# Optimization experiments

Hardware: AMD Instinct MI355X
Metric: run time of the kernel (lower is better)

## Reference

```python
import jax, jax.numpy as jnp
import numpy as np

BN_EPS = 1e-5


def setup_inputs() -> dict:
    N, E, D, L = 100000, 1200000, 64, 3
    key = jax.random.key(0)
    ks = jax.random.split(key, 6)
    x = jax.random.normal(ks[0], (N, D), dtype=jnp.float32)
    src = jax.random.randint(ks[1], (E,), 0, N, dtype=jnp.int32)
    dst = jax.random.randint(ks[2], (E,), 0, N, dtype=jnp.int32)
    W1 = jax.random.normal(ks[3], (L, D, D), dtype=jnp.float32) * 0.1
    W2 = jax.random.normal(ks[4], (L, D, D), dtype=jnp.float32) * 0.1
    b1 = jnp.zeros((L, D), jnp.float32)
    b2 = jnp.zeros((L, D), jnp.float32)
    bn_gamma = jnp.ones((L, D), jnp.float32)
    bn_beta = jnp.zeros((L, D), jnp.float32)
    bn_mean = jnp.zeros((L, D), jnp.float32)
    bn_var = jnp.ones((L, D), jnp.float32)
    return {"x": x, "src": src, "dst": dst, "W1": W1, "b1": b1,
            "bn_gamma": bn_gamma, "bn_beta": bn_beta, "bn_mean": bn_mean,
            "bn_var": bn_var, "W2": W2, "b2": b2}


def reference(x, src, dst, W1, b1, bn_gamma, bn_beta, bn_mean, bn_var, W2, b2):
    # GIN stack, eval mode (dropout is a no-op, BatchNorm uses running stats).
    N = x.shape[0]
    L = W1.shape[0]
    h = x
    jk_sum = jnp.zeros((N, W2.shape[-1]), x.dtype)
    for layer in range(L):  # small fixed layer loop
        # GINConv with eps=0: (1+eps)*x_i + sum_{j->i} x_j
        agg = jax.ops.segment_sum(h[src], dst, num_segments=N)  # [N, D]
        pre = h + agg
        # MLP: Linear -> BatchNorm1d (inference) -> ReLU -> Linear
        z = pre @ W1[layer] + b1[layer]
        z = bn_gamma[layer] * (z - bn_mean[layer]) * jax.lax.rsqrt(bn_var[layer] + BN_EPS) + bn_beta[layer]
        z = jax.nn.relu(z)
        h = z @ W2[layer] + b2[layer]
        if layer != L - 1:
            h = jax.nn.relu(h)  # inter-layer ReLU from the wrapper
        jk_sum = jk_sum + h  # JK='sum' over h_list[1:]
    return jk_sum
```

## Files before the change

kernel.cpp:

```cpp
#include <hip/hip_runtime.h>
#include <hip/hip_fp16.h>

#define NDIM 64
#define RS 68
#define MAXNB 512
#define CAP 6144
#define EBUF 352

typedef _Float16 h4 __attribute__((ext_vector_type(4)));
typedef float f4v __attribute__((ext_vector_type(4)));

__global__ __launch_bounds__(256) void prep_kernel(
    const float* __restrict__ x, __half* __restrict__ x16, int n4,
    const float* __restrict__ W1, const float* __restrict__ b1,
    const float* __restrict__ gamma, const float* __restrict__ beta,
    const float* __restrict__ mean, const float* __restrict__ var,
    const float* __restrict__ W2,
    _Float16* __restrict__ Wpk, float* __restrict__ b1f, int L)
{
    int bid = blockIdx.x;
    int t = threadIdx.x;
    if (bid < 2 * L) {
        int l = bid >> 1, m = bid & 1;
        const float* Wsrc = (m == 0 ? W1 : W2) + (size_t)l * 4096;
        if (m == 0 && t < 64) {
            float s = gamma[l * 64 + t] * rsqrtf(var[l * 64 + t] + 1e-5f);
            b1f[l * 64 + t] = (b1[l * 64 + t] - mean[l * 64 + t]) * s + beta[l * 64 + t];
        }
        int lane = t & 63;
        int c16 = lane & 15, kq = lane >> 4;
        for (int it = 0; it < 4; ++it) {
            int frag = it * 4 + (t >> 6);
            int ks = frag >> 2, ct = frag & 3;
            int col = ct * 16 + c16;
            int k0 = ks * 16 + kq * 4;
            float s = 1.f;
            if (m == 0) s = gamma[l * 64 + col] * rsqrtf(var[l * 64 + col] + 1e-5f);
            _Float16* dstp = Wpk + (((size_t)(l * 2 + m) * 16 + frag) * 64 + lane) * 8;
            for (int j = 0; j < 4; ++j) {
                float wv = Wsrc[(size_t)(k0 + j) * 64 + col] * s;
                _Float16 hi = (_Float16)wv;
                dstp[j] = hi;
                dstp[4 + j] = (_Float16)(wv - (float)hi);
            }
        }
        return;
    }
    int tid = (bid - 2 * L) * 256 + t;
    if (tid >= n4) return;
    float4 v = *(const float4*)(x + (size_t)tid * 4);
    __half2* dp = (__half2*)(x16 + (size_t)tid * 4);
    dp[0] = __floats2half2_rn(v.x, v.y);
    dp[1] = __floats2half2_rn(v.z, v.w);
}

__global__ __launch_bounds__(256) void bucket_scatter_kernel(
    const int* __restrict__ src, const int* __restrict__ dst,
    int* __restrict__ bcnt, unsigned int* __restrict__ packed, int E, int NBb)
{
    __shared__ int hist[MAXNB];
    __shared__ int sbase[MAXNB];
    for (int i = threadIdx.x; i < NBb; i += 256) hist[i] = 0;
    __syncthreads();
    int start = blockIdx.x * blockDim.x + threadIdx.x;
    int stride = gridDim.x * blockDim.x;
    for (int e = start; e < E; e += stride)
        atomicAdd(&hist[dst[e] >> 8], 1);
    __syncthreads();
    for (int i = threadIdx.x; i < NBb; i += 256) {
        int v = hist[i];
        sbase[i] = v ? (i * CAP + atomicAdd(&bcnt[i], v)) : 0;
    }
    __syncthreads();
    for (int i = threadIdx.x; i < NBb; i += 256) hist[i] = 0;
    __syncthreads();
    for (int e = start; e < E; e += stride) {
        int d = dst[e];
        int b = d >> 8;
        int r = atomicAdd(&hist[b], 1);
        packed[sbase[b] + r] = (unsigned)src[e] | ((unsigned)(d & 255) << 24);
    }
}

__global__ __launch_bounds__(256) void bucket_csr_kernel(
    const unsigned int* __restrict__ packed, const int* __restrict__ bcnt,
    int* __restrict__ ssrc, int* __restrict__ offs, int* __restrict__ ends, int N)
{
    __shared__ int hist[256], scan[256], cur[256];
    __shared__ int swbase;
    int b = blockIdx.x;
    int t = threadIdx.x;
    int partial = 0;
    for (int i = t; i < b; i += 256) partial += bcnt[i];
    scan[t] = partial;
    hist[t] = 0;
    __syncthreads();
    for (int d = 128; d > 0; d >>= 1) {
        if (t < d) scan[t] += scan[t + d];
        __syncthreads();
    }
    if (t == 0) swbase = scan[0];
    __syncthreads();
    int wbase = swbase;
    int cnt = bcnt[b];
    if (cnt > CAP) cnt = CAP;
    size_t rbase = (size_t)b * CAP;
    for (int i = t; i < cnt; i += 256)
        atomicAdd(&hist[packed[rbase + i] >> 24], 1);
    __syncthreads();
    int v = hist[t];
    scan[t] = v;
    __syncthreads();
    for (int d = 1; d < 256; d <<= 1) {
        int x = scan[t];
        int y = (t >= d) ? scan[t - d] : 0;
        __syncthreads();
        scan[t] = x + y;
        __syncthreads();
    }
    int e0 = wbase + scan[t] - v;
    cur[t] = e0;
    int node = b * 256 + t;
    if (node < N) { offs[node] = e0; ends[node] = e0 + v; }
    __syncthreads();
    for (int i = t; i < cnt; i += 256) {
        unsigned p = packed[rbase + i];
        int pos = atomicAdd(&cur[p >> 24], 1);
        ssrc[pos] = (int)(p & 0xFFFFFF);
    }
}

__device__ inline void add4(float4& a, const float4& v) {
    a.x += v.x; a.y += v.y; a.z += v.z; a.w += v.w;
}

__device__ inline void cvt_acc(uint4 u, float4& a0, float4& a1) {
    __half2 h0 = __builtin_bit_cast(__half2, u.x);
    __half2 h1 = __builtin_bit_cast(__half2, u.y);
    __half2 h2 = __builtin_bit_cast(__half2, u.z);
    __half2 h3 = __builtin_bit_cast(__half2, u.w);
    float2 f0 = __half22float2(h0), f1 = __half22float2(h1);
    float2 f2 = __half22float2(h2), f3 = __half22float2(h3);
    a0.x += f0.x; a0.y += f0.y; a0.z += f1.x; a0.w += f1.y;
    a1.x += f2.x; a1.y += f2.y; a1.z += f3.x; a1.w += f3.y;
}

__global__ __launch_bounds__(256, 7) void gin_layer_kernel(
    const __half* __restrict__ hin, __half* __restrict__ hout,
    float* __restrict__ jk,
    const int* __restrict__ offs, const int* __restrict__ ends,
    const int* __restrict__ ssrc,
    const _Float16* __restrict__ w1p, const _Float16* __restrict__ w2p,
    const float* __restrict__ b1f, const float* __restrict__ b2,
    int N, int relu_out, int first, int write_h)
{
    __shared__ float lds[64 * RS];
    __shared__ int ebuf_s[4 * EBUF];
    int t = threadIdx.x;
    int lane = t & 63;
    int w = t >> 6;
    int row0 = blockIdx.x * 64;
    int wrow0 = row0 + w * 16;
    if (wrow0 >= N) return;

    float* wtile = lds + (size_t)w * 16 * RS;
    int* ebuf = ebuf_s + w * EBUF;

    int offv = 0, endv = 0;
    if (lane < 16) {
        int node = wrow0 + lane;
        int cn = (node < N) ? node : (N - 1);
        offv = offs[cn];
        endv = ends[cn];
        if (node >= N) offv = endv;
    }
    int begAll = __shfl(offv, 0, 64);
    int endAll = __shfl(endv, 15, 64);
    int cnt = endAll - begAll;

    float4 jpre[4];
    #pragma unroll
    for (int it = 0; it < 4; ++it) jpre[it] = make_float4(0.f, 0.f, 0.f, 0.f);
    if (!first) {
        #pragma unroll
        for (int it = 0; it < 4; ++it) {
            int fl = it * 64 + lane;
            int r = fl >> 4, c4 = fl & 15;
            int grow = wrow0 + r;
            if (grow < N)
                jpre[it] = *(const float4*)(jk + (size_t)grow * NDIM + c4 * 4);
        }
    }

    bool useLds = (cnt <= EBUF);
    if (useLds) {
        for (int k = lane; k < cnt; k += 64) ebuf[k] = ssrc[begAll + k];
    }
    asm volatile("" ::: "memory");
    auto eidx = [&](int pos) -> int {
        return useLds ? ebuf[pos - begAll] : ssrc[pos];
    };

    int rslot = lane >> 3;
    int q = lane & 7;
    #pragma unroll
    for (int i = 0; i < 2; ++i) {
        int rsel = i * 8 + rslot;
        int node = wrow0 + rsel;
        int beg = __shfl(offv, rsel, 64);
        int end = __shfl(endv, rsel, 64);

        float4 a0 = make_float4(0.f, 0.f, 0.f, 0.f);
        float4 a1 = make_float4(0.f, 0.f, 0.f, 0.f);
        float4 b0 = make_float4(0.f, 0.f, 0.f, 0.f);
        float4 b1v = make_float4(0.f, 0.f, 0.f, 0.f);
        if (node < N) {
            uint4 u = *(const uint4*)(hin + (size_t)node * NDIM + q * 8);
            cvt_acc(u, a0, a1);
        }
        int k = beg;
        for (; k + 2 <= end; k += 2) {
            int i0 = eidx(k), i1 = eidx(k + 1);
            uint4 u0 = *(const uint4*)(hin + (size_t)i0 * NDIM + q * 8);
            uint4 u1 = *(const uint4*)(hin + (size_t)i1 * NDIM + q * 8);
            cvt_acc(u0, a0, a1);
            cvt_acc(u1, b0, b1v);
        }
        if (k < end) {
            uint4 u0 = *(const uint4*)(hin + (size_t)eidx(k) * NDIM + q * 8);
            cvt_acc(u0, a0, a1);
        }
        add4(a0, b0); add4(a1, b1v);
        if (node < N) {
            float* p = wtile + rsel * RS + q * 8;
            *(float4*)(p) = a0;
            *(float4*)(p + 4) = a1;
        }
    }
    asm volatile("" ::: "memory");

    int lane15 = lane & 15;
    int lgrp = lane >> 4;
    const float* aRow = wtile + (size_t)lane15 * RS;
    const h4* W1 = (const h4*)w1p;
    const h4* W2 = (const h4*)w2p;
    f4v zero = {0.f, 0.f, 0.f, 0.f};
    f4v acc[4];

    #pragma unroll
    for (int ct = 0; ct < 4; ++ct) acc[ct] = zero;
    #pragma unroll
    for (int ks = 0; ks < 4; ++ks) {
        float4 av = *(const float4*)(aRow + ks * 16 + lgrp * 4);
        h4 ah, al;
        ah[0] = (_Float16)av.x; al[0] = (_Float16)(av.x - (float)ah[0]);
        ah[1] = (_Float16)av.y; al[1] = (_Float16)(av.y - (float)ah[1]);
        ah[2] = (_Float16)av.z; al[2] = (_Float16)(av.z - (float)ah[2]);
        ah[3] = (_Float16)av.w; al[3] = (_Float16)(av.w - (float)ah[3]);
        #pragma unroll
        for (int ct = 0; ct < 4; ++ct) {
            const h4* bp = W1 + (size_t)((ks * 4 + ct) * 64 + lane) * 2;
            h4 bh = bp[0], bl = bp[1];
            acc[ct] = __builtin_amdgcn_mfma_f32_16x16x16f16(ah, bh, acc[ct], 0, 0, 0);
            acc[ct] = __builtin_amdgcn_mfma_f32_16x16x16f16(al, bh, acc[ct], 0, 0, 0);
            acc[ct] = __builtin_amdgcn_mfma_f32_16x16x16f16(ah, bl, acc[ct], 0, 0, 0);
        }
    }
    asm volatile("" ::: "memory");
    #pragma unroll
    for (int ct = 0; ct < 4; ++ct) {
        int col = ct * 16 + lane15;
        float bb = b1f[col];
        #pragma unroll
        for (int i = 0; i < 4; ++i)
            wtile[(size_t)(lgrp * 4 + i) * RS + col] = fmaxf(acc[ct][i] + bb, 0.f);
    }
    asm volatile("" ::: "memory");

    #pragma unroll
    for (int ct = 0; ct < 4; ++ct) acc[ct] = zero;
    #pragma unroll
    for (int ks = 0; ks < 4; ++ks) {
        float4 av = *(const float4*)(aRow + ks * 16 + lgrp * 4);
        h4 ah, al;
        ah[0] = (_Float16)av.x; al[0] = (_Float16)(av.x - (float)ah[0]);
        ah[1] = (_Float16)av.y; al[1] = (_Float16)(av.y - (float)ah[1]);
        ah[2] = (_Float16)av.z; al[2] = (_Float16)(av.z - (float)ah[2]);
        ah[3] = (_Float16)av.w; al[3] = (_Float16)(av.w - (float)ah[3]);
        #pragma unroll
        for (int ct = 0; ct < 4; ++ct) {
            const h4* bp = W2 + (size_t)((ks * 4 + ct) * 64 + lane) * 2;
            h4 bh = bp[0], bl = bp[1];
            acc[ct] = __builtin_amdgcn_mfma_f32_16x16x16f16(ah, bh, acc[ct], 0, 0, 0);
            acc[ct] = __builtin_amdgcn_mfma_f32_16x16x16f16(al, bh, acc[ct], 0, 0, 0);
            acc[ct] = __builtin_amdgcn_mfma_f32_16x16x16f16(ah, bl, acc[ct], 0, 0, 0);
        }
    }
    asm volatile("" ::: "memory");
    #pragma unroll
    for (int ct = 0; ct < 4; ++ct) {
        int col = ct * 16 + lane15;
        float bb = b2[col];
        #pragma unroll
        for (int i = 0; i < 4; ++i) {
            float hv = acc[ct][i] + bb;
            if (relu_out) hv = fmaxf(hv, 0.f);
            wtile[(size_t)(lgrp * 4 + i) * RS + col] = hv;
        }
    }
    asm volatile("" ::: "memory");

    #pragma unroll
    for (int it = 0; it < 4; ++it) {
        int fl = it * 64 + lane;
        int r = fl >> 4, c4 = fl & 15;
        int grow = wrow0 + r;
        if (grow >= N) continue;
        const float* p = wtile + (size_t)r * RS + c4 * 4;
        float4 hv = make_float4(p[0], p[1], p[2], p[3]);
        if (write_h) {
            __half2* dp = (__half2*)(hout + (size_t)grow * NDIM + c4 * 4);
            dp[0] = __floats2half2_rn(hv.x, hv.y);
            dp[1] = __floats2half2_rn(hv.z, hv.w);
        }
        float4 jv;
        if (first) jv = hv;
        else {
            float4 o = jpre[it];
            jv = make_float4(o.x + hv.x, o.y + hv.y, o.z + hv.z, o.w + hv.w);
        }
        *(float4*)(jk + (size_t)grow * NDIM + c4 * 4) = jv;
    }
}

extern "C" void kernel_launch(void* const* d_in, const int* in_sizes, int n_in,
                              void* d_out, int out_size, void* d_ws, size_t ws_size,
                              hipStream_t stream) {
    const float* x     = (const float*)d_in[0];
    const int*   src   = (const int*)  d_in[1];
    const int*   dst   = (const int*)  d_in[2];
    const float* W1    = (const float*)d_in[3];
    const float* b1    = (const float*)d_in[4];
    const float* gamma = (const float*)d_in[5];
    const float* beta  = (const float*)d_in[6];
    const float* mean  = (const float*)d_in[7];
    const float* var   = (const float*)d_in[8];
    const float* W2    = (const float*)d_in[9];
    const float* b2    = (const float*)d_in[10];

    int N = in_sizes[0] / NDIM;
    int E = in_sizes[1];
    int L = in_sizes[3] / (NDIM * NDIM);
    int NBb = (N + 255) >> 8;
    int n4 = N * NDIM / 4;
    float* out = (float*)d_out;

    char* w = (char*)d_ws;
    size_t off = 0;
    auto carve = [&](size_t bytes) -> void* {
        void* p = w + off;
        off += (bytes + 255) & ~(size_t)255;
        return p;
    };
    __half* h16A    = (__half*)carve((size_t)N * NDIM * 2);
    __half* h16B    = (__half*)carve((size_t)N * NDIM * 2);
    int*    ssrc    = (int*)   carve((size_t)E * 4);
    unsigned int* packed = (unsigned int*)carve((size_t)NBb * CAP * 4);
    int*    offs    = (int*)   carve((size_t)N * 4);
    int*    ends    = (int*)   carve((size_t)N * 4);
    int*    bcnt    = (int*)   carve((size_t)(MAXNB + 1) * 4);
    _Float16* Wpk   = (_Float16*)carve((size_t)L * 2 * 16 * 64 * 8 * 2);
    float*  b1f     = (float*) carve((size_t)L * NDIM * 4);

    hipMemsetAsync(bcnt, 0, (size_t)(MAXNB + 1) * 4, stream);
    prep_kernel<<<2 * L + (n4 + 255) / 256, 256, 0, stream>>>(
        x, h16A, n4, W1, b1, gamma, beta, mean, var, W2, Wpk, b1f, L);
    bucket_scatter_kernel<<<256, 256, 0, stream>>>(src, dst, bcnt, packed, E, NBb);
    bucket_csr_kernel<<<NBb, 256, 0, stream>>>(packed, bcnt, ssrc, offs, ends, N);

    const __half* hin = h16A;
    __half* hout = h16B;
    for (int l = 0; l < L; ++l) {
        gin_layer_kernel<<<(N + 63) / 64, 256, 0, stream>>>(
            hin, hout, out, offs, ends, ssrc,
            Wpk + (size_t)(l * 2 + 0) * 16 * 64 * 8,
            Wpk + (size_t)(l * 2 + 1) * 16 * 64 * 8,
            b1f + (size_t)l * NDIM, b2 + (size_t)l * NDIM,
            N, (l < L - 1) ? 1 : 0, (l == 0) ? 1 : 0, (l < L - 1) ? 1 : 0);
        const __half* tmp = hin;
        hin = hout;
        hout = (__half*)tmp;
    }
}
```

Before: 250.4 us.

## Keep per-layer fp16 activations and sum JK output once in last layer

```diff
diff --git a/kernel.cpp b/kernel.cpp
--- a/kernel.cpp
+++ b/kernel.cpp
@@ -16,11 +16,14 @@
     const float* __restrict__ gamma, const float* __restrict__ beta,
     const float* __restrict__ mean, const float* __restrict__ var,
     const float* __restrict__ W2,
-    _Float16* __restrict__ Wpk, float* __restrict__ b1f, int L)
+    _Float16* __restrict__ Wpk, float* __restrict__ b1f, int L,
+    int* __restrict__ bcnt, int nbz)
 {
     int bid = blockIdx.x;
     int t = threadIdx.x;
     if (bid < 2 * L) {
+        if (bid == 0)
+            for (int i = t; i < nbz; i += 256) bcnt[i] = 0;
         int l = bid >> 1, m = bid & 1;
         const float* Wsrc = (m == 0 ? W1 : W2) + (size_t)l * 4096;
         if (m == 0 && t < 64) {
@@ -147,12 +150,12 @@
 
 __global__ __launch_bounds__(256, 7) void gin_layer_kernel(
     const __half* __restrict__ hin, __half* __restrict__ hout,
-    float* __restrict__ jk,
+    float* __restrict__ jk, const __half* __restrict__ hbase,
     const int* __restrict__ offs, const int* __restrict__ ends,
     const int* __restrict__ ssrc,
     const _Float16* __restrict__ w1p, const _Float16* __restrict__ w2p,
     const float* __restrict__ b1f, const float* __restrict__ b2,
-    int N, int relu_out, int first, int write_h)
+    int N, int L, int relu_out, int last)
 {
     __shared__ float lds[64 * RS];
     __shared__ int ebuf_s[4 * EBUF];
@@ -178,20 +181,6 @@
     int endAll = __shfl(endv, 15, 64);
     int cnt = endAll - begAll;
 
-    float4 jpre[4];
-    #pragma unroll
-    for (int it = 0; it < 4; ++it) jpre[it] = make_float4(0.f, 0.f, 0.f, 0.f);
-    if (!first) {
-        #pragma unroll
-        for (int it = 0; it < 4; ++it) {
-            int fl = it * 64 + lane;
-            int r = fl >> 4, c4 = fl & 15;
-            int grow = wrow0 + r;
-            if (grow < N)
-                jpre[it] = *(const float4*)(jk + (size_t)grow * NDIM + c4 * 4);
-        }
-    }
-
     bool useLds = (cnt <= EBUF);
     if (useLds) {
         for (int k = lane; k < cnt; k += 64) ebuf[k] = ssrc[begAll + k];
@@ -201,40 +190,57 @@
         return useLds ? ebuf[pos - begAll] : ssrc[pos];
     };
 
-    int rslot = lane >> 3;
-    int q = lane & 7;
-    #pragma unroll
-    for (int i = 0; i < 2; ++i) {
-        int rsel = i * 8 + rslot;
-        int node = wrow0 + rsel;
-        int beg = __shfl(offv, rsel, 64);
-        int end = __shfl(endv, rsel, 64);
+    {
+        int rslot = lane >> 3;
+        int q = lane & 7;
+        int nodeA = wrow0 + rslot;
+        int nodeB = wrow0 + 8 + rslot;
+        int begA = __shfl(offv, rslot, 64),     endA = __shfl(endv, rslot, 64);
+        int begB = __shfl(offv, 8 + rslot, 64), endB = __shfl(endv, 8 + rslot, 64);
 
         float4 a0 = make_float4(0.f, 0.f, 0.f, 0.f);
         float4 a1 = make_float4(0.f, 0.f, 0.f, 0.f);
-        float4 b0 = make_float4(0.f, 0.f, 0.f, 0.f);
-        float4 b1v = make_float4(0.f, 0.f, 0.f, 0.f);
-        if (node < N) {
-            uint4 u = *(const uint4*)(hin + (size_t)node * NDIM + q * 8);
+        float4 c0 = make_float4(0.f, 0.f, 0.f, 0.f);
+        float4 c1 = make_float4(0.f, 0.f, 0.f, 0.f);
+        if (nodeA < N) {
+            uint4 u = *(const uint4*)(hin + (size_t)nodeA * NDIM + q * 8);
             cvt_acc(u, a0, a1);
         }
-        int k = beg;
-        for (; k + 2 <= end; k += 2) {
-            int i0 = eidx(k), i1 = eidx(k + 1);
-            uint4 u0 = *(const uint4*)(hin + (size_t)i0 * NDIM + q * 8);
-            uint4 u1 = *(const uint4*)(hin + (size_t)i1 * NDIM + q * 8);
-            cvt_acc(u0, a0, a1);
-            cvt_acc(u1, b0, b1v);
-        }
-        if (k < end) {
-            uint4 u0 = *(const uint4*)(hin + (size_t)eidx(k) * NDIM + q * 8);
-            cvt_acc(u0, a0, a1);
-        }
-        add4(a0, b0); add4(a1, b1v);
-        if (node < N) {
-            float* p = wtile + rsel * RS + q * 8;
+        if (nodeB < N) {
+            uint4 u = *(const uint4*)(hin + (size_t)nodeB * NDIM + q * 8);
+            cvt_acc(u, c0, c1);
+        }
+        int kA = begA, kB = begB;
+        while (kA + 2 <= endA && kB + 2 <= endB) {
+            int iA0 = eidx(kA), iA1 = eidx(kA + 1);
+            int iB0 = eidx(kB), iB1 = eidx(kB + 1);
+            uint4 uA0 = *(const uint4*)(hin + (size_t)iA0 * NDIM + q * 8);
+            uint4 uA1 = *(const uint4*)(hin + (size_t)iA1 * NDIM + q * 8);
+            uint4 uB0 = *(const uint4*)(hin + (size_t)iB0 * NDIM + q * 8);
+            uint4 uB1 = *(const uint4*)(hin + (size_t)iB1 * NDIM + q * 8);
+            cvt_acc(uA0, a0, a1);
+            cvt_acc(uA1, a0, a1);
+            cvt_acc(uB0, c0, c1);
+            cvt_acc(uB1, c0, c1);
+            kA += 2; kB += 2;
+        }
+        for (; kA < endA; ++kA) {
+            uint4 u = *(const uint4*)(hin + (size_t)eidx(kA) * NDIM + q * 8);
+            cvt_acc(u, a0, a1);
+        }
+        for (; kB < endB; ++kB) {
+            uint4 u = *(const uint4*)(hin + (size_t)eidx(kB) * NDIM + q * 8);
+            cvt_acc(u, c0, c1);
+        }
+        if (nodeA < N) {
+            float* p = wtile + rslot * RS + q * 8;
             *(float4*)(p) = a0;
             *(float4*)(p + 4) = a1;
+        }
+        if (nodeB < N) {
+            float* p = wtile + (8 + rslot) * RS + q * 8;
+            *(float4*)(p) = c0;
+            *(float4*)(p + 4) = c1;
         }
     }
     asm volatile("" ::: "memory");
@@ -310,6 +316,7 @@
     }
     asm volatile("" ::: "memory");
 
+    size_t nstride = (size_t)N * NDIM;
     #pragma unroll
     for (int it = 0; it < 4; ++it) {
         int fl = it * 64 + lane;
@@ -318,18 +325,21 @@
         if (grow >= N) continue;
         const float* p = wtile + (size_t)r * RS + c4 * 4;
         float4 hv = make_float4(p[0], p[1], p[2], p[3]);
-        if (write_h) {
+        if (!last) {
             __half2* dp = (__half2*)(hout + (size_t)grow * NDIM + c4 * 4);
             dp[0] = __floats2half2_rn(hv.x, hv.y);
             dp[1] = __floats2half2_rn(hv.z, hv.w);
-        }
-        float4 jv;
-        if (first) jv = hv;
-        else {
-            float4 o = jpre[it];
-            jv = make_float4(o.x + hv.x, o.y + hv.y, o.z + hv.z, o.w + hv.w);
-        }
-        *(float4*)(jk + (size_t)grow * NDIM + c4 * 4) = jv;
+        } else {
+            for (int j = 1; j < L; ++j) {
+                uint2 u = *(const uint2*)(hbase + (size_t)j * nstride
+                                          + (size_t)grow * NDIM + c4 * 4);
+                __half2 x0 = __builtin_bit_cast(__half2, u.x);
+                __half2 x1 = __builtin_bit_cast(__half2, u.y);
+                float2 f0 = __half22float2(x0), f1 = __half22float2(x1);
+                hv.x += f0.x; hv.y += f0.y; hv.z += f1.x; hv.w += f1.y;
+            }
+            *(float4*)(jk + (size_t)grow * NDIM + c4 * 4) = hv;
+        }
     }
 }
 
@@ -354,6 +364,7 @@
     int NBb = (N + 255) >> 8;
     int n4 = N * NDIM / 4;
     float* out = (float*)d_out;
+    size_t ns = (size_t)N * NDIM;
 
     char* w = (char*)d_ws;
     size_t off = 0;
@@ -362,8 +373,7 @@
         off += (bytes + 255) & ~(size_t)255;
         return p;
     };
-    __half* h16A    = (__half*)carve((size_t)N * NDIM * 2);
-    __half* h16B    = (__half*)carve((size_t)N * NDIM * 2);
+    __half* h16     = (__half*)carve((size_t)(L + 1) * ns * 2);
     int*    ssrc    = (int*)   carve((size_t)E * 4);
     unsigned int* packed = (unsigned int*)carve((size_t)NBb * CAP * 4);
     int*    offs    = (int*)   carve((size_t)N * 4);
@@ -372,23 +382,19 @@
     _Float16* Wpk   = (_Float16*)carve((size_t)L * 2 * 16 * 64 * 8 * 2);
     float*  b1f     = (float*) carve((size_t)L * NDIM * 4);
 
-    hipMemsetAsync(bcnt, 0, (size_t)(MAXNB + 1) * 4, stream);
     prep_kernel<<<2 * L + (n4 + 255) / 256, 256, 0, stream>>>(
-        x, h16A, n4, W1, b1, gamma, beta, mean, var, W2, Wpk, b1f, L);
+        x, h16, n4, W1, b1, gamma, beta, mean, var, W2, Wpk, b1f, L,
+        bcnt, NBb + 1);
     bucket_scatter_kernel<<<256, 256, 0, stream>>>(src, dst, bcnt, packed, E, NBb);
     bucket_csr_kernel<<<NBb, 256, 0, stream>>>(packed, bcnt, ssrc, offs, ends, N);
 
-    const __half* hin = h16A;
-    __half* hout = h16B;
     for (int l = 0; l < L; ++l) {
         gin_layer_kernel<<<(N + 63) / 64, 256, 0, stream>>>(
-            hin, hout, out, offs, ends, ssrc,
+            h16 + (size_t)l * ns, h16 + (size_t)(l + 1) * ns, out, h16,
+            offs, ends, ssrc,
             Wpk + (size_t)(l * 2 + 0) * 16 * 64 * 8,
             Wpk + (size_t)(l * 2 + 1) * 16 * 64 * 8,
             b1f + (size_t)l * NDIM, b2 + (size_t)l * NDIM,
-            N, (l < L - 1) ? 1 : 0, (l == 0) ? 1 : 0, (l < L - 1) ? 1 : 0);
-        const __half* tmp = hin;
-        hin = hout;
-        hout = (__half*)tmp;
-    }
-}
+            N, L, (l < L - 1) ? 1 : 0, (l == L - 1) ? 1 : 0);
+    }
+}
```

After: 244.4 us. 2.4% less time.
